# Optimization experiments

Measured on AMD Instinct MI355X. Metric: run time of the kernel, lower is better.

The kernel has to match this reference:

```python
import jax, jax.numpy as jnp
import numpy as np

B, N, M = 2, 512, 8192
DIM, CTX, H, DH, MULT = 1024, 512, 16, 64, 4
INNER = H * DH


def layernorm(x, scale, bias, eps=1e-5):
    mu = x.mean(-1, keepdims=True)
    var = ((x - mu) ** 2).mean(-1, keepdims=True)
    return (x - mu) / jnp.sqrt(var + eps) * scale + bias


def rotate_half(x):
    # interleaved pairs: (..., d) -> (..., d/2, 2), (x1, x2) -> (-x2, x1)
    xr = x.reshape(x.shape[:-1] + (-1, 2))
    x1, x2 = xr[..., 0], xr[..., 1]
    return jnp.stack((-x2, x1), axis=-1).reshape(x.shape)


def apply_rope(freqs, x):
    # freqs: [b, seq, dh] -> [b, 1, seq, dh]; x: [b, h, seq, dh]
    f = freqs[:, None, :, :]
    return x * jnp.cos(f) + rotate_half(x) * jnp.sin(f)


def setup_inputs() -> dict:
    key = jax.random.key(0)
    ks = jax.random.split(key, 24)
    s = 0.02
    inp = {
        "x_query": jax.random.normal(ks[0], (B, N, DIM), jnp.float32),
        "x_context": jax.random.normal(ks[1], (B, M, CTX), jnp.float32),
        "rope_q": jax.random.normal(ks[2], (B, N, DH), jnp.float32),
        "rope_ctx": jax.random.normal(ks[3], (B, M, DH), jnp.float32),
        "Wq": jax.random.normal(ks[4], (DIM, INNER), jnp.float32) * s,
        "Wkv": jax.random.normal(ks[5], (CTX, 2 * INNER), jnp.float32) * s,
        "Wo": jax.random.normal(ks[6], (INNER, DIM), jnp.float32) * s,
        "bo": jnp.zeros((DIM,), jnp.float32),
        "ln_q_scale": jnp.ones((DIM,), jnp.float32),
        "ln_q_bias": jnp.zeros((DIM,), jnp.float32),
        "ln_c_scale": jnp.ones((CTX,), jnp.float32),
        "ln_c_bias": jnp.zeros((CTX,), jnp.float32),
        "ffn_ln_scale": jnp.ones((DIM,), jnp.float32),
        "ffn_ln_bias": jnp.zeros((DIM,), jnp.float32),
        "W1": jax.random.normal(ks[7], (DIM, DIM * MULT * 2), jnp.float32) * s,
        "b1": jnp.zeros((DIM * MULT * 2,), jnp.float32),
        "W2": jax.random.normal(ks[8], (DIM * MULT, DIM), jnp.float32) * s,
        "b2": jnp.zeros((DIM,), jnp.float32),
        "attn_mask": jnp.ones((B, M), dtype=bool),
    }
    return inp


def reference(x_query, x_context, rope_q, rope_ctx, Wq, Wkv, Wo, bo,
              ln_q_scale, ln_q_bias, ln_c_scale, ln_c_bias,
              ffn_ln_scale, ffn_ln_bias, W1, b1, W2, b2, attn_mask):
    # --- RotaryCrossAttention ---
    hq = layernorm(x_query, ln_q_scale, ln_q_bias)
    hc = layernorm(x_context, ln_c_scale, ln_c_bias)
    q = (hq @ Wq).reshape(B, N, H, DH).transpose(0, 2, 1, 3)          # b h n d
    kv = hc @ Wkv
    k = kv[..., :INNER].reshape(B, M, H, DH).transpose(0, 2, 1, 3)    # b h m d
    v = kv[..., INNER:].reshape(B, M, H, DH).transpose(0, 2, 1, 3)
    q = apply_rope(rope_q, q)
    k = apply_rope(rope_ctx, k)
    v = apply_rope(rope_ctx, v)  # rotate_value=True
    scale = DH ** -0.5
    scores = jnp.einsum('bhnd,bhmd->bhnm', q, k) * scale
    scores = jnp.where(attn_mask[:, None, None, :], scores, -1e9)
    attn = jax.nn.softmax(scores, axis=-1)
    out = jnp.einsum('bhnm,bhmd->bhnd', attn, v)
    out = apply_rope(-rope_q, out)  # un-rotate values
    out = out.transpose(0, 2, 1, 3).reshape(B, N, INNER)
    out = out @ Wo + bo
    res = x_query + out
    # --- pre-norm GEGLU FeedForward ---
    y = layernorm(res, ffn_ln_scale, ffn_ln_bias)
    u = y @ W1 + b1
    a, g = u[..., :DIM * MULT], u[..., DIM * MULT:]
    z = (a * jax.nn.gelu(g, approximate=False)) @ W2 + b2
    return res + z
```

## Files before the change

kernel.cpp:

```cpp
#include <hip/hip_runtime.h>
#include <hip/hip_bf16.h>
#include <math.h>


typedef __bf16 bf16;
typedef __bf16 bf16x8 __attribute__((ext_vector_type(8)));
typedef float f32x4 __attribute__((ext_vector_type(4)));

#define DEVI static __device__ __forceinline__

union BV {
  uint4 u;
  bf16 b[8];
  bf16x8 v;
};

DEVI float bf2f(bf16 x) { return (float)x; }
DEVI bf16 f2bf(float x) { return (bf16)x; }

DEVI void gload16(const void* g, void* l) {
  __builtin_amdgcn_global_load_lds((const __attribute__((address_space(1))) void*)g,
                                   (__attribute__((address_space(3))) void*)l, 16, 0, 0);
}

// ... 102 lines not shown
    if constexpr (EPI == 7) {
      const int b = bn >> 2;
      const int nblk = (bn & 3) * 128;
#pragma unroll
      for (int it = 0; it < 8; it++) {
        const int id = it * 256 + tid;
        const int hl = id >> 10, rem = id & 1023;
        const int mm = rem >> 3, c = rem & 7;
        const uint4 vv = *(const uint4*)(ot + mm * 272 + hl * 128 + c * 16);
        const int hg = bm * 2 + hl;
        *(uint4*)((bf16*)out0 + ((size_t)(b * 16 + hg) * 512 + nblk + mm) * 64 + c * 8) = vv;
      }
    } else {
      const int b = bn >> 6;
      const int mblk = (bn & 63) * 128;
      if (isK) {
#pragma unroll
        for (int it = 0; it < 8; it++) {
          const int id = it * 256 + tid;
          const int hl = id >> 10, rem = id & 1023;
          const int mm = rem >> 3, c = rem & 7;
          const uint4 vv = *(const uint4*)(ot + mm * 272 + hl * 128 + c * 16);
          const int hg = bm * 2 + hl;
          *(uint4*)((bf16*)out0 + ((size_t)(b * 16 + hg) * 8192 + mblk + mm) * 64 + c * 8) = vv;
        }
      } else {
#pragma unroll
        for (int it = 0; it < 8; it++) {
          const int id = it * 256 + tid;
          const int nl = id >> 4, c = id & 15;
          const uint4 vv = *(const uint4*)(ot + nl * 272 + c * 16);
          const int hg = (bm - 8) * 2 + (nl >> 6);
          const int d = nl & 63;
          *(uint4*)((bf16*)out1 + ((size_t)(b * 16 + hg) * 64 + d) * 8192 + mblk + c * 8) = vv;
        }
      }
    }
  } else {
#pragma unroll
    for (int fm = 0; fm < 4; fm++) {
#pragma unroll
      for (int fn = 0; fn < 4; fn++) {
        const int col = bn * 128 + wn * 64 + fn * 16 + ln15;
#pragma unroll
        for (int j = 0; j < 4; j++) {
          const int row = bm * 128 + wm * 64 + fm * 16 + lh * 4 + j;
          ((bf16*)out0)[((size_t)zidx * Mdim + row) * Ndim + col] = f2bf(acc[fm][fn][j]);
        }
      }
    }
  }
}

__global__ __launch_bounds__(256, 2)
void gemm128_p(const bf16* __restrict__ A, const bf16* __restrict__ Bt,
               int Mdim, int Ndim, int Kdim,
               void* __restrict__ out0) {
  extern __shared__ char smem[];
  const int kpz = Kdim / gridDim.z;
  gemm_body<6>(smem, blockIdx.x, blockIdx.y, blockIdx.z * kpz, kpz, blockIdx.z,
               A, Bt, Mdim, Ndim, Kdim, nullptr, out0, nullptr);
}

__global__ __launch_bounds__(256, 2)
void gemm_kvq(const bf16* __restrict__ WkvT, const bf16* __restrict__ hc,
              const float* __restrict__ cs, bf16* __restrict__ k_buf,
              bf16* __restrict__ v_t, const bf16* __restrict__ hq,
              const bf16* __restrict__ WqT, const float* __restrict__ csq,
              bf16* __restrict__ q_buf) {
  extern __shared__ char smem[];
  const int fid = blockIdx.x;
  if (fid < 64) {
    gemm_body<7>(smem, fid >> 3, fid & 7, 0, 1024, 0,
                 WqT, hq, 1024, 1024, 1024, csq, q_buf, nullptr);
  } else {
    const int t = fid - 64;
    const int bn = (t & 7) * 16 + ((t >> 3) & 15);
    const int bm = t >> 7;
    gemm_body<5>(smem, bm, bn, 0, 512, 0, WkvT, hc, 2048, 16384, 512, cs, k_buf, v_t);
  }
}

__global__ __launch_bounds__(256, 4)
void gemm_geglu(const bf16* __restrict__ A, const bf16* __restrict__ Bt,
                const float* __restrict__ b1, bf16* __restrict__ hg) {
  __shared__ bf16 As[64 * 64];
  __shared__ bf16 Bs[128 * 64];
  const int tid = threadIdx.x;
  const int w = tid >> 6, l = tid & 63;
  const int bm = blockIdx.x, bn = blockIdx.y;
  const int ln15 = l & 15, lh = l >> 4;
  const int sw7 = ln15 & 7;

  const int gcol = ((l & 7) ^ ((l >> 3) & 7)) << 3;
  const bf16* aG = A + (size_t)(bm * 64 + w * 16 + (l >> 3)) * 1024 + gcol;
  bf16* lA = As + (w * 16) * 64;
  const bf16* bG = Bt + (size_t)((w >> 1) * 4096 + bn * 64 + ((w & 1) * 32 + (l >> 3))) * 1024 + gcol;
  bf16* lB = Bs + (w * 32) * 64;

  const f32x4 z4 = {0.f, 0.f, 0.f, 0.f};
  f32x4 acc[2][4];
#pragma unroll
  for (int p = 0; p < 2; p++)
#pragma unroll
    for (int i = 0; i < 4; i++) acc[p][i] = z4;

  const char* Ab = (const char*)As;
  const char* Bb = (const char*)Bs;
  const int arow_b = ln15 * 128;

  for (int k0 = 0; k0 < 1024; k0 += 64) {
#pragma unroll
    for (int gi = 0; gi < 2; gi++)
      gload16(aG + (size_t)(gi * 8) * 1024 + k0, lA + gi * 512);
#pragma unroll
    for (int gi = 0; gi < 4; gi++)
      gload16(bG + (size_t)(gi * 8) * 1024 + k0, lB + gi * 512);
    __syncthreads();
#pragma unroll
    for (int kk = 0; kk < 2; kk++) {
      const int gx = (((kk << 2) | lh) ^ sw7) << 4;
      bf16x8 af[4], bfr[2];
#pragma unroll
      for (int f = 0; f < 4; f++) {
        BV t0;
        t0.u = *(const uint4*)(Ab + arow_b + f * 2048 + gx);
        af[f] = t0.v;
      }
#pragma unroll
      for (int p = 0; p < 2; p++) {
        const int cu = p * 64 + w * 16 + ln15;
        BV t0;
        t0.u = *(const uint4*)(Bb + cu * 128 + gx);
        bfr[p] = t0.v;
      }
#pragma unroll
      for (int fm = 0; fm < 4; fm++)
#pragma unroll
        for (int p = 0; p < 2; p++)
          acc[p][fm] = __builtin_amdgcn_mfma_f32_16x16x32_bf16(af[fm], bfr[p], acc[p][fm], 0, 0, 0);
    }
    __syncthreads();
  }

  const int col = bn * 64 + w * 16 + ln15;
  const float ba = b1[col], bg = b1[4096 + col];
#pragma unroll
  for (int fm = 0; fm < 4; fm++) {
#pragma unroll
    for (int j = 0; j < 4; j++) {
      const int row = bm * 64 + fm * 16 + lh * 4 + j;
      const float a = acc[0][fm][j] + ba;
      const float g = acc[1][fm][j] + bg;
      const float ge = 0.5f * g * (1.f + erff(g * 0.70710678118f));
      hg[(size_t)row * 4096 + col] = f2bf(a * ge);
    }
  }
}

template <int S>
__global__ __launch_bounds__(256)
void combine_res_ln(const bf16* __restrict__ part, const float* __restrict__ bias,
                    const float* __restrict__ resid, float* __restrict__ out,
                    const float* __restrict__ lnsc, const float* __restrict__ lnbi,
                    bf16* __restrict__ yout) {
  __shared__ float r0[4], r1[4];
  const int row = blockIdx.x, tid = threadIdx.x;
  const int wv = tid >> 6, l = tid & 63;
  const size_t i4 = (size_t)row * 1024 + tid * 4;
  const int col = tid * 4;
  float4 s = {0.f, 0.f, 0.f, 0.f};
#pragma unroll
  for (int p = 0; p < S; p++) {
    union { uint2 u; bf16 bb[4]; } t;
    t.u = *(const uint2*)(part + (size_t)p * 1048576 + i4);
    s.x += bf2f(t.bb[0]); s.y += bf2f(t.bb[1]);
    s.z += bf2f(t.bb[2]); s.w += bf2f(t.bb[3]);
  }
  const float4 bv = *(const float4*)(bias + col);
  const float4 rv = *(const float4*)(resid + i4);
  s.x += bv.x + rv.x; s.y += bv.y + rv.y; s.z += bv.z + rv.z; s.w += bv.w + rv.w;
  *(float4*)(out + i4) = s;
  float sm = s.x + s.y + s.z + s.w;
  float ss = s.x * s.x + s.y * s.y + s.z * s.z + s.w * s.w;
#pragma unroll
  for (int off = 1; off < 64; off <<= 1) { sm += __shfl_xor(sm, off); ss += __shfl_xor(ss, off); }
  if (l == 0) { r0[wv] = sm; r1[wv] = ss; }
  __syncthreads();
  sm = r0[0] + r0[1] + r0[2] + r0[3];
  ss = r1[0] + r1[1] + r1[2] + r1[3];
  const float mu = sm * (1.f / 1024.f);
  const float rstd = rsqrtf(ss * (1.f / 1024.f) - mu * mu + 1e-5f);
  const float4 scv = *(const float4*)(lnsc + col);
  const float4 biv = *(const float4*)(lnbi + col);
  union { uint2 u; bf16 bb[4]; } y;
  y.bb[0] = f2bf((s.x - mu) * rstd * scv.x + biv.x);
  y.bb[1] = f2bf((s.y - mu) * rstd * scv.y + biv.y);
  y.bb[2] = f2bf((s.z - mu) * rstd * scv.z + biv.z);
  y.bb[3] = f2bf((s.w - mu) * rstd * scv.w + biv.w);
  *(uint2*)(yout + i4) = y.u;
}

template <int S>
__global__ __launch_bounds__(256)
void combine_res_bf16(const bf16* __restrict__ part, const float* __restrict__ bias,
                      const float* __restrict__ resid, float* __restrict__ out) {
  const size_t i4 = ((size_t)blockIdx.x * 256 + threadIdx.x) * 4;
  float4 s = {0.f, 0.f, 0.f, 0.f};
#pragma unroll
  for (int p = 0; p < S; p++) {
    union { uint2 u; bf16 bb[4]; } t;
    t.u = *(const uint2*)(part + (size_t)p * 1048576 + i4);
    s.x += bf2f(t.bb[0]); s.y += bf2f(t.bb[1]);
    s.z += bf2f(t.bb[2]); s.w += bf2f(t.bb[3]);
  }
  const int col = (int)(i4 & 1023);
  const float4 bv = *(const float4*)(bias + col);
  const float4 rv = *(const float4*)(resid + i4);
  s.x += bv.x + rv.x; s.y += bv.y + rv.y; s.z += bv.z + rv.z; s.w += bv.w + rv.w;
  *(float4*)(out + i4) = s;
}

__global__ __launch_bounds__(256, 4)
void attn_kernel(const bf16* __restrict__ q_buf, const bf16* __restrict__ k_buf,
                 const bf16* __restrict__ v_t, bf16* __restrict__ opart,
                 float* __restrict__ lpart) {
  __shared__ bf16 Ks[2][64 * 64];
  __shared__ bf16 Vs[2][64 * 64];
  __shared__ bf16 Ps[4][16][64];
  const int id = blockIdx.x;
  const int sp = id >> 7, qt = (id >> 5) & 3, bh = id & 31;
  const int tid = threadIdx.x;
  const int w = tid >> 6, l = tid & 63;
  const int ln15 = l & 15, lh = l >> 4;

  const bf16* qbase = q_buf + ((size_t)bh * 512 + qt * 128 + w * 32) * 64;
  const bf16* kbase = k_buf + (size_t)bh * 8192 * 64;
  const bf16* vbase = v_t + (size_t)bh * 64 * 8192;

  bf16x8 aq[2][2];
#pragma unroll
  for (int rh = 0; rh < 2; rh++) {
    const bf16* qp = qbase + (size_t)(rh * 16 + ln15) * 64 + lh * 8;
    BV t0; t0.u = *(const uint4*)qp; aq[rh][0] = t0.v;
    BV t1; t1.u = *(const uint4*)(qp + 32); aq[rh][1] = t1.v;
  }

  const f32x4 z4 = {0.f, 0.f, 0.f, 0.f};
  f32x4 o[2][4];
#pragma unroll
  for (int rh = 0; rh < 2; rh++)
#pragma unroll
    for (int fd = 0; fd < 4; fd++) o[rh][fd] = z4;
  f32x4 ol[2] = {z4, z4};

  BV ones;
#pragma unroll
  for (int i = 0; i < 8; i++) ones.b[i] = f2bf(1.0f);

  const int srow0 = ((w << 1) | 0) * 8 + (l >> 3);
  const int srow1 = ((w << 1) | 1) * 8 + (l >> 3);
  const int slot = l & 7;
  const int g0 = (slot ^ (srow0 & 7)) << 3;
  const int g1 = (slot ^ (srow1 & 7)) << 3;
  const bf16* k0p = kbase + (size_t)srow0 * 64 + g0;
  const bf16* k1p = kbase + (size_t)srow1 * 64 + g1;
  const bf16* v0p = vbase + (size_t)srow0 * 8192 + g0;
  const bf16* v1p = vbase + (size_t)srow1 * 8192 + g1;
  const int lo0 = ((w << 1) | 0) * 512;
  const int lo1 = ((w << 1) | 1) * 512;

  const int mt0 = sp * 16;
  auto STAGE = [&](int b, int mt) {
    const size_t mo = (size_t)mt * 4096;
    const size_t mv = (size_t)mt * 64;
    gload16(k0p + mo, Ks[b] + lo0);
    gload16(k1p + mo, Ks[b] + lo1);
    gload16(v0p + mv, Vs[b] + lo0);
    gload16(v1p + mv, Vs[b] + lo1);
  };

  STAGE(0, mt0);
  __syncthreads();

  char* pbase = (char*)&Ps[w][0][0];
  const int swq = ln15 & 7;

  for (int i = 0; i < 16; i++) {
    const int cur = i & 1;
    if (i < 15) STAGE(cur ^ 1, mt0 + i + 1);

    const char* Kb = (const char*)Ks[cur];
    const char* Vb = (const char*)Vs[cur];

    f32x4 sf[2][4];
#pragma unroll
    for (int rh = 0; rh < 2; rh++)
#pragma unroll
      for (int fn = 0; fn < 4; fn++) sf[rh][fn] = z4;
    __builtin_amdgcn_s_setprio(1);
#pragma unroll
    for (int fn = 0; fn < 4; fn++) {
      const int mrow = fn * 16 + ln15;
      const int sw = mrow & 7;
      BV t0; t0.u = *(const uint4*)(Kb + mrow * 128 + ((lh ^ sw) << 4));
      BV t1; t1.u = *(const uint4*)(Kb + mrow * 128 + (((lh + 4) ^ sw) << 4));
      sf[0][fn] = __builtin_amdgcn_mfma_f32_16x16x32_bf16(t0.v, aq[0][0], sf[0][fn], 0, 0, 0);
      sf[0][fn] = __builtin_amdgcn_mfma_f32_16x16x32_bf16(t1.v, aq[0][1], sf[0][fn], 0, 0, 0);
      sf[1][fn] = __builtin_amdgcn_mfma_f32_16x16x32_bf16(t0.v, aq[1][0], sf[1][fn], 0, 0, 0);
      sf[1][fn] = __builtin_amdgcn_mfma_f32_16x16x32_bf16(t1.v, aq[1][1], sf[1][fn], 0, 0, 0);
    }
    __builtin_amdgcn_s_setprio(0);

    BV pa[2][2];
#pragma unroll
    for (int rh = 0; rh < 2; rh++) {
      char* prow = pbase + ln15 * 128;
#pragma unroll
      for (int fn = 0; fn < 4; fn++) {
        const float p0 = exp2f(sf[rh][fn][0]);
        const float p1 = exp2f(sf[rh][fn][1]);
        const float p2 = exp2f(sf[rh][fn][2]);
        const float p3 = exp2f(sf[rh][fn][3]);
        union { uint2 u; bf16 bb[4]; } pk;
        pk.bb[0] = f2bf(p0); pk.bb[1] = f2bf(p1);
        pk.bb[2] = f2bf(p2); pk.bb[3] = f2bf(p3);
        const int G = (fn * 2 + (lh >> 1)) ^ swq;
        *(uint2*)(prow + G * 16 + (lh & 1) * 8) = pk.u;
      }
#pragma unroll
      for (int mh = 0; mh < 2; mh++) {
        const int R = ((mh << 2) | lh) ^ swq;
        pa[rh][mh].u = *(const uint4*)(pbase + ln15 * 128 + (R << 4));
      }
    }

    __builtin_amdgcn_s_setprio(1);
#pragma unroll
    for (int mh = 0; mh < 2; mh++) {
      ol[0] = __builtin_amdgcn_mfma_f32_16x16x32_bf16(pa[0][mh].v, ones.v, ol[0], 0, 0, 0);
      ol[1] = __builtin_amdgcn_mfma_f32_16x16x32_bf16(pa[1][mh].v, ones.v, ol[1], 0, 0, 0);
#pragma unroll
      for (int fd = 0; fd < 4; fd++) {
        const int drow = fd * 16 + ln15;
        BV bv; bv.u = *(const uint4*)(Vb + drow * 128 + ((((mh << 2) | lh) ^ (drow & 7)) << 4));
        o[0][fd] = __builtin_amdgcn_mfma_f32_16x16x32_bf16(pa[0][mh].v, bv.v, o[0][fd], 0, 0, 0);
        o[1][fd] = __builtin_amdgcn_mfma_f32_16x16x32_bf16(pa[1][mh].v, bv.v, o[1][fd], 0, 0, 0);
      }
    }
    __builtin_amdgcn_s_setprio(0);
    __syncthreads();
  }

#pragma unroll
  for (int rh = 0; rh < 2; rh++) {
    if (ln15 == 0) {
#pragma unroll
      for (int j = 0; j < 4; j++)
        lpart[(size_t)id * 128 + w * 32 + rh * 16 + lh * 4 + j] = ol[rh][j];
    }
    bf16* op = opart + (size_t)id * 8192 + (w * 32 + rh * 16) * 64;
#pragma unroll
    for (int fd = 0; fd < 4; fd++)
#pragma unroll
      for (int j = 0; j < 4; j++)
        op[(lh * 4 + j) * 64 + fd * 16 + ln15] = f2bf(o[rh][fd][j]);
  }
}

DEVI void tr_tile(bf16 (*t)[74], const float* __restrict__ in, bf16* __restrict__ out,
                  int R, int C, int ct, int rt, int tid) {
  const int tr = tid >> 2, tc = (tid & 3) << 4;
  {
    const float* src = in + (size_t)(rt * 64 + tr) * C + ct * 64 + tc;
    const float4 a0 = *(const float4*)src;
    const float4 a1 = *(const float4*)(src + 4);
    const float4 a2 = *(const float4*)(src + 8);
    const float4 a3 = *(const float4*)(src + 12);
    t[tr][tc + 0] = f2bf(a0.x);  t[tr][tc + 1] = f2bf(a0.y);
    t[tr][tc + 2] = f2bf(a0.z);  t[tr][tc + 3] = f2bf(a0.w);
    t[tr][tc + 4] = f2bf(a1.x);  t[tr][tc + 5] = f2bf(a1.y);
    t[tr][tc + 6] = f2bf(a1.z);  t[tr][tc + 7] = f2bf(a1.w);
    t[tr][tc + 8] = f2bf(a2.x);  t[tr][tc + 9] = f2bf(a2.y);
    t[tr][tc + 10] = f2bf(a2.z); t[tr][tc + 11] = f2bf(a2.w);
    t[tr][tc + 12] = f2bf(a3.x); t[tr][tc + 13] = f2bf(a3.y);
    t[tr][tc + 14] = f2bf(a3.z); t[tr][tc + 15] = f2bf(a3.w);
  }
  __syncthreads();
  {
    BV a0, a1;
#pragma unroll
    for (int i = 0; i < 8; i++) { a0.b[i] = t[tc + i][tr]; a1.b[i] = t[tc + 8 + i][tr]; }
    bf16* dst = out + (size_t)(ct * 64 + tr) * R + rt * 64 + tc;
    *(uint4*)dst = a0.u;
    *(uint4*)(dst + 8) = a1.u;
  }
}

__global__ __launch_bounds__(256)
void combine_tr_kernel(const bf16* __restrict__ opart, const float* __restrict__ lpart,
                       const float* __restrict__ ct_, const float* __restrict__ st_,
                       bf16* __restrict__ o_lin,
                       const float* __restrict__ W1, bf16* __restrict__ W1T,
                       const float* __restrict__ W2, bf16* __restrict__ W2T) {
  int id = blockIdx.x;
  if (id < 1024) {
    const size_t i4 = ((size_t)id * 256 + threadIdx.x) * 4;
    const int d4 = (int)(i4 & 63);
    const int row = (int)(i4 >> 6);
    const int qg = row & 511;
    const int bh = row >> 9;
    const int qt = qg >> 7, ql = qg & 127;
    const int id0 = (qt << 5) | bh;
    float4 acc = {0.f, 0.f, 0.f, 0.f};
    float L = 0.f;
#pragma unroll
    for (int sp = 0; sp < 8; sp++) {
      const int pid = (sp << 7) | id0;
      union { uint2 u; bf16 bb[4]; } t;
      t.u = *(const uint2*)(opart + (size_t)pid * 8192 + ql * 64 + d4);
      acc.x += bf2f(t.bb[0]); acc.y += bf2f(t.bb[1]);
      acc.z += bf2f(t.bb[2]); acc.w += bf2f(t.bb[3]);
      L += lpart[(size_t)pid * 128 + ql];
    }
    const float inv = 1.f / L;
    const float x0 = acc.x * inv, x1 = acc.y * inv, x2 = acc.z * inv, x3 = acc.w * inv;
    const int b = bh >> 4, h = bh & 15, n = qg;
    const size_t fo = (((size_t)b * 512 + n) * 64) + d4;
    const float4 cv = *(const float4*)(ct_ + fo);
    const float4 sv = *(const float4*)(st_ + fo);
    union { uint2 u; bf16 bb[4]; } o;
    o.bb[0] = f2bf(x0 * cv.x + x1 * sv.x);
    o.bb[1] = f2bf(x1 * cv.y - x0 * sv.y);
    o.bb[2] = f2bf(x2 * cv.z + x3 * sv.z);
    o.bb[3] = f2bf(x3 * cv.w - x2 * sv.w);
    *(uint2*)(o_lin + (((size_t)b * 512 + n) * 1024) + h * 64 + d4) = o.u;
  } else {
    __shared__ bf16 t[64][74];
    id -= 1024;
    if (id < 2048) {
      tr_tile(t, W1, W1T, 1024, 8192, id & 127, id >> 7, threadIdx.x);
    } else {
      id -= 2048;
      tr_tile(t, W2, W2T, 4096, 1024, id & 15, id >> 4, threadIdx.x);
    }
  }
}

template <int W>
DEVI void ln_row(const float* __restrict__ xr, const float* __restrict__ sc,
                 const float* __restrict__ bi, bf16* __restrict__ outr,
                 int tid, float* r0, float* r1) {
  constexpr int PER = W / 256;
  const int w = tid >> 6, l = tid & 63;
  float v[PER];
  if constexpr (PER == 4) {
    const float4 t = *(const float4*)(xr + tid * 4);
    v[0] = t.x; v[1] = t.y; v[2] = t.z; v[3] = t.w;
  } else {
    const float2 t = *(const float2*)(xr + tid * 2);
    v[0] = t.x; v[1] = t.y;
  }
  float s = 0.f, ss = 0.f;
#pragma unroll
  for (int i = 0; i < PER; i++) { s += v[i]; ss += v[i] * v[i]; }
#pragma unroll
  for (int off = 1; off < 64; off <<= 1) { s += __shfl_xor(s, off); ss += __shfl_xor(ss, off); }
  if (l == 0) { r0[w] = s; r1[w] = ss; }
  __syncthreads();
  s = r0[0] + r0[1] + r0[2] + r0[3];
  ss = r1[0] + r1[1] + r1[2] + r1[3];
  const float mu = s * (1.f / W);
  const float rstd = rsqrtf(ss * (1.f / W) - mu * mu + 1e-5f);
  if constexpr (PER == 4) {
    union { uint2 u; bf16 b[4]; } t;
#pragma unroll
    for (int i = 0; i < 4; i++) {
      const int c = tid * 4 + i;
      t.b[i] = f2bf((v[i] - mu) * rstd * sc[c] + bi[c]);
    }
    *(uint2*)(outr + tid * 4) = t.u;
  } else {
    union { unsigned u; bf16 b[2]; } t;
#pragma unroll
    for (int i = 0; i < 2; i++) {
      const int c = tid * 2 + i;
      t.b[i] = f2bf((v[i] - mu) * rstd * sc[c] + bi[c]);
    }
    *(unsigned*)(outr + tid * 2) = t.u;
  }
}

__global__ __launch_bounds__(256)
void setup_kernel(const float* __restrict__ Wq, bf16* __restrict__ WqT,
                  const float* __restrict__ Wkv, bf16* __restrict__ WkvT,
                  const float* __restrict__ Wo, bf16* __restrict__ WoT,
                  const float* __restrict__ fq, float* __restrict__ cq,
                  float* __restrict__ sq_, unsigned* __restrict__ csq,
                  const float* __restrict__ fc, unsigned* __restrict__ cs,
// ... 70 lines not shown
  const float* lnf_s = (const float*)d_in[12];
  const float* lnf_b = (const float*)d_in[13];
  const float* W1 = (const float*)d_in[14];
  const float* b1 = (const float*)d_in[15];
  const float* W2 = (const float*)d_in[16];
  const float* b2 = (const float*)d_in[17];

  char* ws = (char*)d_ws;
  size_t off = 0;
  auto alloc = [&](size_t bytes) {
    char* p = ws + off;
    off += (bytes + 255) & ~(size_t)255;
    return p;
  };

  bf16* WqT = (bf16*)alloc((size_t)1048576 * 2);
  bf16* WkvT = (bf16*)alloc((size_t)1048576 * 2);
  bf16* WoT = (bf16*)alloc((size_t)1048576 * 2);
  bf16* hq = (bf16*)alloc((size_t)1048576 * 2);
  bf16* q_buf = (bf16*)alloc((size_t)1048576 * 2);
  float* cosq = (float*)alloc((size_t)65536 * 4);
  float* sinq = (float*)alloc((size_t)65536 * 4);
  unsigned* csq = (unsigned*)alloc((size_t)65536 * 4);
  unsigned* cs_ctx = (unsigned*)alloc((size_t)1048576 * 4);
  bf16* o_lin = (bf16*)alloc((size_t)1048576 * 2);
  float* res = (float*)alloc((size_t)1048576 * 4);
  bf16* ybuf = (bf16*)alloc((size_t)1048576 * 2);
  float* lpart = (float*)alloc((size_t)131072 * 4);
  bf16* hc = (bf16*)alloc((size_t)8388608 * 2);
  bf16* k_buf = (bf16*)alloc((size_t)16777216 * 2);
  bf16* W1T = k_buf;
  bf16* W2T = k_buf + 8388608;
  bf16* hg = k_buf + 8388608 + 4194304;
  char* regB = alloc((size_t)16777216 * 2);
  bf16* opart = (bf16*)regB;
  bf16* pwo = (bf16*)regB;
  bf16* pf2 = (bf16*)regB;
  bf16* v_tb = (bf16*)alloc((size_t)16777216 * 2);
  (void)ws_size;

  const int SH = 32768;
  const int SH5 = 34816;

  setup_kernel<<<22528, 256, 0, stream>>>(Wq, WqT, Wkv, WkvT, Wo, WoT,
                                          rope_q, cosq, sinq, csq, rope_ctx, cs_ctx,
                                          x_query, lnq_s, lnq_b, hq,
                                          x_context, lnc_s, lnc_b, hc);

  gemm_kvq<<<2112, 256, SH5, stream>>>(WkvT, hc, (const float*)cs_ctx,
                                       k_buf, v_tb, hq, WqT,
                                       (const float*)csq, q_buf);

  attn_kernel<<<1024, 256, 0, stream>>>(q_buf, k_buf, v_tb, opart, lpart);
  combine_tr_kernel<<<4096, 256, 0, stream>>>(opart, lpart, cosq, sinq, o_lin,
                                              W1, W1T, W2, W2T);

  gemm128_p<<<dim3(8, 8, 4), 256, SH, stream>>>(o_lin, WoT, 1024, 1024, 1024, pwo);
  combine_res_ln<4><<<1024, 256, 0, stream>>>(pwo, bo, x_query, res, lnf_s, lnf_b, ybuf);

  gemm_geglu<<<dim3(16, 64), 256, 0, stream>>>(ybuf, W1T, b1, hg);
  gemm128_p<<<dim3(8, 8, 8), 256, SH, stream>>>(hg, W2T, 1024, 1024, 4096, pf2);
  combine_res_bf16<8><<<1024, 256, 0, stream>>>(pf2, b2, res, (float*)d_out);
}
```

Baseline: 206.7 us.

## Move W1/W2 transposes from attention combine into split-K Wo GEMM launch

```diff
diff --git a/kernel.cpp b/kernel.cpp
--- a/kernel.cpp
+++ b/kernel.cpp
@@ -178,322 +178,6 @@
   }
 }
 
-__global__ __launch_bounds__(256, 2)
-void gemm128_p(const bf16* __restrict__ A, const bf16* __restrict__ Bt,
-               int Mdim, int Ndim, int Kdim,
-               void* __restrict__ out0) {
-  extern __shared__ char smem[];
-  const int kpz = Kdim / gridDim.z;
-  gemm_body<6>(smem, blockIdx.x, blockIdx.y, blockIdx.z * kpz, kpz, blockIdx.z,
-               A, Bt, Mdim, Ndim, Kdim, nullptr, out0, nullptr);
-}
-
-__global__ __launch_bounds__(256, 2)
-void gemm_kvq(const bf16* __restrict__ WkvT, const bf16* __restrict__ hc,
-              const float* __restrict__ cs, bf16* __restrict__ k_buf,
-              bf16* __restrict__ v_t, const bf16* __restrict__ hq,
-              const bf16* __restrict__ WqT, const float* __restrict__ csq,
-              bf16* __restrict__ q_buf) {
-  extern __shared__ char smem[];
-  const int fid = blockIdx.x;
-  if (fid < 64) {
-    gemm_body<7>(smem, fid >> 3, fid & 7, 0, 1024, 0,
-                 WqT, hq, 1024, 1024, 1024, csq, q_buf, nullptr);
-  } else {
-    const int t = fid - 64;
-    const int bn = (t & 7) * 16 + ((t >> 3) & 15);
-    const int bm = t >> 7;
-    gemm_body<5>(smem, bm, bn, 0, 512, 0, WkvT, hc, 2048, 16384, 512, cs, k_buf, v_t);
-  }
-}
-
-__global__ __launch_bounds__(256, 4)
-void gemm_geglu(const bf16* __restrict__ A, const bf16* __restrict__ Bt,
-                const float* __restrict__ b1, bf16* __restrict__ hg) {
-  __shared__ bf16 As[64 * 64];
-  __shared__ bf16 Bs[128 * 64];
-  const int tid = threadIdx.x;
-  const int w = tid >> 6, l = tid & 63;
-  const int bm = blockIdx.x, bn = blockIdx.y;
-  const int ln15 = l & 15, lh = l >> 4;
-  const int sw7 = ln15 & 7;
-
-  const int gcol = ((l & 7) ^ ((l >> 3) & 7)) << 3;
-  const bf16* aG = A + (size_t)(bm * 64 + w * 16 + (l >> 3)) * 1024 + gcol;
-  bf16* lA = As + (w * 16) * 64;
-  const bf16* bG = Bt + (size_t)((w >> 1) * 4096 + bn * 64 + ((w & 1) * 32 + (l >> 3))) * 1024 + gcol;
-  bf16* lB = Bs + (w * 32) * 64;
-
-  const f32x4 z4 = {0.f, 0.f, 0.f, 0.f};
-  f32x4 acc[2][4];
-#pragma unroll
-  for (int p = 0; p < 2; p++)
-#pragma unroll
-    for (int i = 0; i < 4; i++) acc[p][i] = z4;
-
-  const char* Ab = (const char*)As;
-  const char* Bb = (const char*)Bs;
-  const int arow_b = ln15 * 128;
-
-  for (int k0 = 0; k0 < 1024; k0 += 64) {
-#pragma unroll
-    for (int gi = 0; gi < 2; gi++)
-      gload16(aG + (size_t)(gi * 8) * 1024 + k0, lA + gi * 512);
-#pragma unroll
-    for (int gi = 0; gi < 4; gi++)
-      gload16(bG + (size_t)(gi * 8) * 1024 + k0, lB + gi * 512);
-    __syncthreads();
-#pragma unroll
-    for (int kk = 0; kk < 2; kk++) {
-      const int gx = (((kk << 2) | lh) ^ sw7) << 4;
-      bf16x8 af[4], bfr[2];
-#pragma unroll
-      for (int f = 0; f < 4; f++) {
-        BV t0;
-        t0.u = *(const uint4*)(Ab + arow_b + f * 2048 + gx);
-        af[f] = t0.v;
-      }
-#pragma unroll
-      for (int p = 0; p < 2; p++) {
-        const int cu = p * 64 + w * 16 + ln15;
-        BV t0;
-        t0.u = *(const uint4*)(Bb + cu * 128 + gx);
-        bfr[p] = t0.v;
-      }
-#pragma unroll
-      for (int fm = 0; fm < 4; fm++)
-#pragma unroll
-        for (int p = 0; p < 2; p++)
-          acc[p][fm] = __builtin_amdgcn_mfma_f32_16x16x32_bf16(af[fm], bfr[p], acc[p][fm], 0, 0, 0);
-    }
-    __syncthreads();
-  }
-
-  const int col = bn * 64 + w * 16 + ln15;
-  const float ba = b1[col], bg = b1[4096 + col];
-#pragma unroll
-  for (int fm = 0; fm < 4; fm++) {
-#pragma unroll
-    for (int j = 0; j < 4; j++) {
-      const int row = bm * 64 + fm * 16 + lh * 4 + j;
-      const float a = acc[0][fm][j] + ba;
-      const float g = acc[1][fm][j] + bg;
-      const float ge = 0.5f * g * (1.f + erff(g * 0.70710678118f));
-      hg[(size_t)row * 4096 + col] = f2bf(a * ge);
-    }
-  }
-}
-
-template <int S>
-__global__ __launch_bounds__(256)
-void combine_res_ln(const bf16* __restrict__ part, const float* __restrict__ bias,
-                    const float* __restrict__ resid, float* __restrict__ out,
-                    const float* __restrict__ lnsc, const float* __restrict__ lnbi,
-                    bf16* __restrict__ yout) {
-  __shared__ float r0[4], r1[4];
-  const int row = blockIdx.x, tid = threadIdx.x;
-  const int wv = tid >> 6, l = tid & 63;
-  const size_t i4 = (size_t)row * 1024 + tid * 4;
-  const int col = tid * 4;
-  float4 s = {0.f, 0.f, 0.f, 0.f};
-#pragma unroll
-  for (int p = 0; p < S; p++) {
-    union { uint2 u; bf16 bb[4]; } t;
-    t.u = *(const uint2*)(part + (size_t)p * 1048576 + i4);
-    s.x += bf2f(t.bb[0]); s.y += bf2f(t.bb[1]);
-    s.z += bf2f(t.bb[2]); s.w += bf2f(t.bb[3]);
-  }
-  const float4 bv = *(const float4*)(bias + col);
-  const float4 rv = *(const float4*)(resid + i4);
-  s.x += bv.x + rv.x; s.y += bv.y + rv.y; s.z += bv.z + rv.z; s.w += bv.w + rv.w;
-  *(float4*)(out + i4) = s;
-  float sm = s.x + s.y + s.z + s.w;
-  float ss = s.x * s.x + s.y * s.y + s.z * s.z + s.w * s.w;
-#pragma unroll
-  for (int off = 1; off < 64; off <<= 1) { sm += __shfl_xor(sm, off); ss += __shfl_xor(ss, off); }
-  if (l == 0) { r0[wv] = sm; r1[wv] = ss; }
-  __syncthreads();
-  sm = r0[0] + r0[1] + r0[2] + r0[3];
-  ss = r1[0] + r1[1] + r1[2] + r1[3];
-  const float mu = sm * (1.f / 1024.f);
-  const float rstd = rsqrtf(ss * (1.f / 1024.f) - mu * mu + 1e-5f);
-  const float4 scv = *(const float4*)(lnsc + col);
-  const float4 biv = *(const float4*)(lnbi + col);
-  union { uint2 u; bf16 bb[4]; } y;
-  y.bb[0] = f2bf((s.x - mu) * rstd * scv.x + biv.x);
-  y.bb[1] = f2bf((s.y - mu) * rstd * scv.y + biv.y);
-  y.bb[2] = f2bf((s.z - mu) * rstd * scv.z + biv.z);
-  y.bb[3] = f2bf((s.w - mu) * rstd * scv.w + biv.w);
-  *(uint2*)(yout + i4) = y.u;
-}
-
-template <int S>
-__global__ __launch_bounds__(256)
-void combine_res_bf16(const bf16* __restrict__ part, const float* __restrict__ bias,
-                      const float* __restrict__ resid, float* __restrict__ out) {
-  const size_t i4 = ((size_t)blockIdx.x * 256 + threadIdx.x) * 4;
-  float4 s = {0.f, 0.f, 0.f, 0.f};
-#pragma unroll
-  for (int p = 0; p < S; p++) {
-    union { uint2 u; bf16 bb[4]; } t;
-    t.u = *(const uint2*)(part + (size_t)p * 1048576 + i4);
-    s.x += bf2f(t.bb[0]); s.y += bf2f(t.bb[1]);
-    s.z += bf2f(t.bb[2]); s.w += bf2f(t.bb[3]);
-  }
-  const int col = (int)(i4 & 1023);
-  const float4 bv = *(const float4*)(bias + col);
-  const float4 rv = *(const float4*)(resid + i4);
-  s.x += bv.x + rv.x; s.y += bv.y + rv.y; s.z += bv.z + rv.z; s.w += bv.w + rv.w;
-  *(float4*)(out + i4) = s;
-}
-
-__global__ __launch_bounds__(256, 4)
-void attn_kernel(const bf16* __restrict__ q_buf, const bf16* __restrict__ k_buf,
-                 const bf16* __restrict__ v_t, bf16* __restrict__ opart,
-                 float* __restrict__ lpart) {
-  __shared__ bf16 Ks[2][64 * 64];
-  __shared__ bf16 Vs[2][64 * 64];
-  __shared__ bf16 Ps[4][16][64];
-  const int id = blockIdx.x;
-  const int sp = id >> 7, qt = (id >> 5) & 3, bh = id & 31;
-  const int tid = threadIdx.x;
-  const int w = tid >> 6, l = tid & 63;
-  const int ln15 = l & 15, lh = l >> 4;
-
-  const bf16* qbase = q_buf + ((size_t)bh * 512 + qt * 128 + w * 32) * 64;
-  const bf16* kbase = k_buf + (size_t)bh * 8192 * 64;
-  const bf16* vbase = v_t + (size_t)bh * 64 * 8192;
-
-  bf16x8 aq[2][2];
-#pragma unroll
-  for (int rh = 0; rh < 2; rh++) {
-    const bf16* qp = qbase + (size_t)(rh * 16 + ln15) * 64 + lh * 8;
-    BV t0; t0.u = *(const uint4*)qp; aq[rh][0] = t0.v;
-    BV t1; t1.u = *(const uint4*)(qp + 32); aq[rh][1] = t1.v;
-  }
-
-  const f32x4 z4 = {0.f, 0.f, 0.f, 0.f};
-  f32x4 o[2][4];
-#pragma unroll
-  for (int rh = 0; rh < 2; rh++)
-#pragma unroll
-    for (int fd = 0; fd < 4; fd++) o[rh][fd] = z4;
-  f32x4 ol[2] = {z4, z4};
-
-  BV ones;
-#pragma unroll
-  for (int i = 0; i < 8; i++) ones.b[i] = f2bf(1.0f);
-
-  const int srow0 = ((w << 1) | 0) * 8 + (l >> 3);
-  const int srow1 = ((w << 1) | 1) * 8 + (l >> 3);
-  const int slot = l & 7;
-  const int g0 = (slot ^ (srow0 & 7)) << 3;
-  const int g1 = (slot ^ (srow1 & 7)) << 3;
-  const bf16* k0p = kbase + (size_t)srow0 * 64 + g0;
-  const bf16* k1p = kbase + (size_t)srow1 * 64 + g1;
-  const bf16* v0p = vbase + (size_t)srow0 * 8192 + g0;
-  const bf16* v1p = vbase + (size_t)srow1 * 8192 + g1;
-  const int lo0 = ((w << 1) | 0) * 512;
-  const int lo1 = ((w << 1) | 1) * 512;
-
-  const int mt0 = sp * 16;
-  auto STAGE = [&](int b, int mt) {
-    const size_t mo = (size_t)mt * 4096;
-    const size_t mv = (size_t)mt * 64;
-    gload16(k0p + mo, Ks[b] + lo0);
-    gload16(k1p + mo, Ks[b] + lo1);
-    gload16(v0p + mv, Vs[b] + lo0);
-    gload16(v1p + mv, Vs[b] + lo1);
-  };
-
-  STAGE(0, mt0);
-  __syncthreads();
-
-  char* pbase = (char*)&Ps[w][0][0];
-  const int swq = ln15 & 7;
-
-  for (int i = 0; i < 16; i++) {
-    const int cur = i & 1;
-    if (i < 15) STAGE(cur ^ 1, mt0 + i + 1);
-
-    const char* Kb = (const char*)Ks[cur];
-    const char* Vb = (const char*)Vs[cur];
-
-    f32x4 sf[2][4];
-#pragma unroll
-    for (int rh = 0; rh < 2; rh++)
-#pragma unroll
-      for (int fn = 0; fn < 4; fn++) sf[rh][fn] = z4;
-    __builtin_amdgcn_s_setprio(1);
-#pragma unroll
-    for (int fn = 0; fn < 4; fn++) {
-      const int mrow = fn * 16 + ln15;
-      const int sw = mrow & 7;
-      BV t0; t0.u = *(const uint4*)(Kb + mrow * 128 + ((lh ^ sw) << 4));
-      BV t1; t1.u = *(const uint4*)(Kb + mrow * 128 + (((lh + 4) ^ sw) << 4));
-      sf[0][fn] = __builtin_amdgcn_mfma_f32_16x16x32_bf16(t0.v, aq[0][0], sf[0][fn], 0, 0, 0);
-      sf[0][fn] = __builtin_amdgcn_mfma_f32_16x16x32_bf16(t1.v, aq[0][1], sf[0][fn], 0, 0, 0);
-      sf[1][fn] = __builtin_amdgcn_mfma_f32_16x16x32_bf16(t0.v, aq[1][0], sf[1][fn], 0, 0, 0);
-      sf[1][fn] = __builtin_amdgcn_mfma_f32_16x16x32_bf16(t1.v, aq[1][1], sf[1][fn], 0, 0, 0);
-    }
-    __builtin_amdgcn_s_setprio(0);
-
-    BV pa[2][2];
-#pragma unroll
-    for (int rh = 0; rh < 2; rh++) {
-      char* prow = pbase + ln15 * 128;
-#pragma unroll
-      for (int fn = 0; fn < 4; fn++) {
-        const float p0 = exp2f(sf[rh][fn][0]);
-        const float p1 = exp2f(sf[rh][fn][1]);
-        const float p2 = exp2f(sf[rh][fn][2]);
-        const float p3 = exp2f(sf[rh][fn][3]);
-        union { uint2 u; bf16 bb[4]; } pk;
-        pk.bb[0] = f2bf(p0); pk.bb[1] = f2bf(p1);
-        pk.bb[2] = f2bf(p2); pk.bb[3] = f2bf(p3);
-        const int G = (fn * 2 + (lh >> 1)) ^ swq;
-        *(uint2*)(prow + G * 16 + (lh & 1) * 8) = pk.u;
-      }
-#pragma unroll
-      for (int mh = 0; mh < 2; mh++) {
-        const int R = ((mh << 2) | lh) ^ swq;
-        pa[rh][mh].u = *(const uint4*)(pbase + ln15 * 128 + (R << 4));
-      }
-    }
-
-    __builtin_amdgcn_s_setprio(1);
-#pragma unroll
-    for (int mh = 0; mh < 2; mh++) {
-      ol[0] = __builtin_amdgcn_mfma_f32_16x16x32_bf16(pa[0][mh].v, ones.v, ol[0], 0, 0, 0);
-      ol[1] = __builtin_amdgcn_mfma_f32_16x16x32_bf16(pa[1][mh].v, ones.v, ol[1], 0, 0, 0);
-#pragma unroll
-      for (int fd = 0; fd < 4; fd++) {
-        const int drow = fd * 16 + ln15;
-        BV bv; bv.u = *(const uint4*)(Vb + drow * 128 + ((((mh << 2) | lh) ^ (drow & 7)) << 4));
-        o[0][fd] = __builtin_amdgcn_mfma_f32_16x16x32_bf16(pa[0][mh].v, bv.v, o[0][fd], 0, 0, 0);
-        o[1][fd] = __builtin_amdgcn_mfma_f32_16x16x32_bf16(pa[1][mh].v, bv.v, o[1][fd], 0, 0, 0);
-      }
-    }
-    __builtin_amdgcn_s_setprio(0);
-    __syncthreads();
-  }
-
-#pragma unroll
-  for (int rh = 0; rh < 2; rh++) {
-    if (ln15 == 0) {
-#pragma unroll
-      for (int j = 0; j < 4; j++)
-        lpart[(size_t)id * 128 + w * 32 + rh * 16 + lh * 4 + j] = ol[rh][j];
-    }
-    bf16* op = opart + (size_t)id * 8192 + (w * 32 + rh * 16) * 64;
-#pragma unroll
-    for (int fd = 0; fd < 4; fd++)
-#pragma unroll
-      for (int j = 0; j < 4; j++)
-        op[(lh * 4 + j) * 64 + fd * 16 + ln15] = f2bf(o[rh][fd][j]);
-  }
-}
-
 DEVI void tr_tile(bf16 (*t)[74], const float* __restrict__ in, bf16* __restrict__ out,
                   int R, int C, int ct, int rt, int tid) {
   const int tr = tid >> 2, tc = (tid & 3) << 4;
@@ -523,54 +207,379 @@
   }
 }
 
+__global__ __launch_bounds__(256, 2)
+void gemm_kvq(const bf16* __restrict__ WkvT, const bf16* __restrict__ hc,
+              const float* __restrict__ cs, bf16* __restrict__ k_buf,
+              bf16* __restrict__ v_t, const bf16* __restrict__ hq,
+              const bf16* __restrict__ WqT, const float* __restrict__ csq,
+              bf16* __restrict__ q_buf) {
+  extern __shared__ char smem[];
+  const int fid = blockIdx.x;
+  if (fid < 64) {
+    gemm_body<7>(smem, fid >> 3, fid & 7, 0, 1024, 0,
+                 WqT, hq, 1024, 1024, 1024, csq, q_buf, nullptr);
+  } else {
+    const int t = fid - 64;
+    const int bn = (t & 7) * 16 + ((t >> 3) & 15);
+    const int bm = t >> 7;
+    gemm_body<5>(smem, bm, bn, 0, 512, 0, WkvT, hc, 2048, 16384, 512, cs, k_buf, v_t);
+  }
+}
+
+__global__ __launch_bounds__(256, 2)
+void gemm_wo_tr(const bf16* __restrict__ o_lin, const bf16* __restrict__ WoT,
+                bf16* __restrict__ pwo,
+                const float* __restrict__ W1, bf16* __restrict__ W1T,
+                const float* __restrict__ W2, bf16* __restrict__ W2T) {
+  extern __shared__ char smem[];
+  int fid = blockIdx.x;
+  if (fid < 512) {
+    const int z = fid >> 6, bm = (fid >> 3) & 7, bn = fid & 7;
+    gemm_body<6>(smem, bm, bn, z * 128, 128, z,
+                 o_lin, WoT, 1024, 1024, 1024, nullptr, pwo, nullptr);
+  } else {
+    bf16 (*t)[74] = (bf16(*)[74])smem;
+    fid -= 512;
+    if (fid < 2048) {
+      tr_tile(t, W1, W1T, 1024, 8192, fid & 127, fid >> 7, threadIdx.x);
+    } else {
+      fid -= 2048;
+      tr_tile(t, W2, W2T, 4096, 1024, fid & 15, fid >> 4, threadIdx.x);
+    }
+  }
+}
+
+__global__ __launch_bounds__(256, 2)
+void gemm128_p(const bf16* __restrict__ A, const bf16* __restrict__ Bt,
+               int Mdim, int Ndim, int Kdim,
+               void* __restrict__ out0) {
+  extern __shared__ char smem[];
+  const int kpz = Kdim / gridDim.z;
+  gemm_body<6>(smem, blockIdx.x, blockIdx.y, blockIdx.z * kpz, kpz, blockIdx.z,
+               A, Bt, Mdim, Ndim, Kdim, nullptr, out0, nullptr);
+}
+
+__global__ __launch_bounds__(256, 4)
+void gemm_geglu(const bf16* __restrict__ A, const bf16* __restrict__ Bt,
+                const float* __restrict__ b1, bf16* __restrict__ hg) {
+  __shared__ bf16 As[64 * 64];
+  __shared__ bf16 Bs[128 * 64];
+  const int tid = threadIdx.x;
+  const int w = tid >> 6, l = tid & 63;
+  const int bm = blockIdx.x, bn = blockIdx.y;
+  const int ln15 = l & 15, lh = l >> 4;
+  const int sw7 = ln15 & 7;
+
+  const int gcol = ((l & 7) ^ ((l >> 3) & 7)) << 3;
+  const bf16* aG = A + (size_t)(bm * 64 + w * 16 + (l >> 3)) * 1024 + gcol;
+  bf16* lA = As + (w * 16) * 64;
+  const bf16* bG = Bt + (size_t)((w >> 1) * 4096 + bn * 64 + ((w & 1) * 32 + (l >> 3))) * 1024 + gcol;
+  bf16* lB = Bs + (w * 32) * 64;
+
+  const f32x4 z4 = {0.f, 0.f, 0.f, 0.f};
+  f32x4 acc[2][4];
+#pragma unroll
+  for (int p = 0; p < 2; p++)
+#pragma unroll
+    for (int i = 0; i < 4; i++) acc[p][i] = z4;
+
+  const char* Ab = (const char*)As;
+  const char* Bb = (const char*)Bs;
+  const int arow_b = ln15 * 128;
+
+  for (int k0 = 0; k0 < 1024; k0 += 64) {
+#pragma unroll
+    for (int gi = 0; gi < 2; gi++)
+      gload16(aG + (size_t)(gi * 8) * 1024 + k0, lA + gi * 512);
+#pragma unroll
+    for (int gi = 0; gi < 4; gi++)
+      gload16(bG + (size_t)(gi * 8) * 1024 + k0, lB + gi * 512);
+    __syncthreads();
+#pragma unroll
+    for (int kk = 0; kk < 2; kk++) {
+      const int gx = (((kk << 2) | lh) ^ sw7) << 4;
+      bf16x8 af[4], bfr[2];
+#pragma unroll
+      for (int f = 0; f < 4; f++) {
+        BV t0;
+        t0.u = *(const uint4*)(Ab + arow_b + f * 2048 + gx);
+        af[f] = t0.v;
+      }
+#pragma unroll
+      for (int p = 0; p < 2; p++) {
+        const int cu = p * 64 + w * 16 + ln15;
+        BV t0;
+        t0.u = *(const uint4*)(Bb + cu * 128 + gx);
+        bfr[p] = t0.v;
+      }
+#pragma unroll
+      for (int fm = 0; fm < 4; fm++)
+#pragma unroll
+        for (int p = 0; p < 2; p++)
+          acc[p][fm] = __builtin_amdgcn_mfma_f32_16x16x32_bf16(af[fm], bfr[p], acc[p][fm], 0, 0, 0);
+    }
+    __syncthreads();
+  }
+
+  const int col = bn * 64 + w * 16 + ln15;
+  const float ba = b1[col], bg = b1[4096 + col];
+#pragma unroll
+  for (int fm = 0; fm < 4; fm++) {
+#pragma unroll
+    for (int j = 0; j < 4; j++) {
+      const int row = bm * 64 + fm * 16 + lh * 4 + j;
+      const float a = acc[0][fm][j] + ba;
+      const float g = acc[1][fm][j] + bg;
+      const float ge = 0.5f * g * (1.f + erff(g * 0.70710678118f));
+      hg[(size_t)row * 4096 + col] = f2bf(a * ge);
+    }
+  }
+}
+
+template <int S>
 __global__ __launch_bounds__(256)
-void combine_tr_kernel(const bf16* __restrict__ opart, const float* __restrict__ lpart,
-                       const float* __restrict__ ct_, const float* __restrict__ st_,
-                       bf16* __restrict__ o_lin,
-                       const float* __restrict__ W1, bf16* __restrict__ W1T,
-                       const float* __restrict__ W2, bf16* __restrict__ W2T) {
-  int id = blockIdx.x;
-  if (id < 1024) {
-    const size_t i4 = ((size_t)id * 256 + threadIdx.x) * 4;
-    const int d4 = (int)(i4 & 63);
-    const int row = (int)(i4 >> 6);
-    const int qg = row & 511;
-    const int bh = row >> 9;
-    const int qt = qg >> 7, ql = qg & 127;
-    const int id0 = (qt << 5) | bh;
-    float4 acc = {0.f, 0.f, 0.f, 0.f};
-    float L = 0.f;
-#pragma unroll
-    for (int sp = 0; sp < 8; sp++) {
-      const int pid = (sp << 7) | id0;
-      union { uint2 u; bf16 bb[4]; } t;
-      t.u = *(const uint2*)(opart + (size_t)pid * 8192 + ql * 64 + d4);
-      acc.x += bf2f(t.bb[0]); acc.y += bf2f(t.bb[1]);
-      acc.z += bf2f(t.bb[2]); acc.w += bf2f(t.bb[3]);
-      L += lpart[(size_t)pid * 128 + ql];
-    }
-    const float inv = 1.f / L;
-    const float x0 = acc.x * inv, x1 = acc.y * inv, x2 = acc.z * inv, x3 = acc.w * inv;
-    const int b = bh >> 4, h = bh & 15, n = qg;
-    const size_t fo = (((size_t)b * 512 + n) * 64) + d4;
-    const float4 cv = *(const float4*)(ct_ + fo);
-    const float4 sv = *(const float4*)(st_ + fo);
-    union { uint2 u; bf16 bb[4]; } o;
-    o.bb[0] = f2bf(x0 * cv.x + x1 * sv.x);
-    o.bb[1] = f2bf(x1 * cv.y - x0 * sv.y);
-    o.bb[2] = f2bf(x2 * cv.z + x3 * sv.z);
-    o.bb[3] = f2bf(x3 * cv.w - x2 * sv.w);
-    *(uint2*)(o_lin + (((size_t)b * 512 + n) * 1024) + h * 64 + d4) = o.u;
-  } else {
-    __shared__ bf16 t[64][74];
-    id -= 1024;
-    if (id < 2048) {
-      tr_tile(t, W1, W1T, 1024, 8192, id & 127, id >> 7, threadIdx.x);
-    } else {
-      id -= 2048;
-      tr_tile(t, W2, W2T, 4096, 1024, id & 15, id >> 4, threadIdx.x);
-    }
-  }
+void combine_res_ln(const bf16* __restrict__ part, const float* __restrict__ bias,
+                    const float* __restrict__ resid, float* __restrict__ out,
+                    const float* __restrict__ lnsc, const float* __restrict__ lnbi,
+                    bf16* __restrict__ yout) {
+  __shared__ float r0[4], r1[4];
+  const int row = blockIdx.x, tid = threadIdx.x;
+  const int wv = tid >> 6, l = tid & 63;
+  const size_t i4 = (size_t)row * 1024 + tid * 4;
+  const int col = tid * 4;
+  float4 s = {0.f, 0.f, 0.f, 0.f};
+#pragma unroll
+  for (int p = 0; p < S; p++) {
+    union { uint2 u; bf16 bb[4]; } t;
+    t.u = *(const uint2*)(part + (size_t)p * 1048576 + i4);
+    s.x += bf2f(t.bb[0]); s.y += bf2f(t.bb[1]);
+    s.z += bf2f(t.bb[2]); s.w += bf2f(t.bb[3]);
+  }
+  const float4 bv = *(const float4*)(bias + col);
+  const float4 rv = *(const float4*)(resid + i4);
+  s.x += bv.x + rv.x; s.y += bv.y + rv.y; s.z += bv.z + rv.z; s.w += bv.w + rv.w;
+  *(float4*)(out + i4) = s;
+  float sm = s.x + s.y + s.z + s.w;
+  float ss = s.x * s.x + s.y * s.y + s.z * s.z + s.w * s.w;
+#pragma unroll
+  for (int off = 1; off < 64; off <<= 1) { sm += __shfl_xor(sm, off); ss += __shfl_xor(ss, off); }
+  if (l == 0) { r0[wv] = sm; r1[wv] = ss; }
+  __syncthreads();
+  sm = r0[0] + r0[1] + r0[2] + r0[3];
+  ss = r1[0] + r1[1] + r1[2] + r1[3];
+  const float mu = sm * (1.f / 1024.f);
+  const float rstd = rsqrtf(ss * (1.f / 1024.f) - mu * mu + 1e-5f);
+  const float4 scv = *(const float4*)(lnsc + col);
+  const float4 biv = *(const float4*)(lnbi + col);
+  union { uint2 u; bf16 bb[4]; } y;
+  y.bb[0] = f2bf((s.x - mu) * rstd * scv.x + biv.x);
+  y.bb[1] = f2bf((s.y - mu) * rstd * scv.y + biv.y);
+  y.bb[2] = f2bf((s.z - mu) * rstd * scv.z + biv.z);
+  y.bb[3] = f2bf((s.w - mu) * rstd * scv.w + biv.w);
+  *(uint2*)(yout + i4) = y.u;
+}
+
+template <int S>
+__global__ __launch_bounds__(256)
+void combine_res_bf16(const bf16* __restrict__ part, const float* __restrict__ bias,
+                      const float* __restrict__ resid, float* __restrict__ out) {
+  const size_t i4 = ((size_t)blockIdx.x * 256 + threadIdx.x) * 4;
+  float4 s = {0.f, 0.f, 0.f, 0.f};
+#pragma unroll
+  for (int p = 0; p < S; p++) {
+    union { uint2 u; bf16 bb[4]; } t;
+    t.u = *(const uint2*)(part + (size_t)p * 1048576 + i4);
+    s.x += bf2f(t.bb[0]); s.y += bf2f(t.bb[1]);
+    s.z += bf2f(t.bb[2]); s.w += bf2f(t.bb[3]);
+  }
+  const int col = (int)(i4 & 1023);
+  const float4 bv = *(const float4*)(bias + col);
+  const float4 rv = *(const float4*)(resid + i4);
+  s.x += bv.x + rv.x; s.y += bv.y + rv.y; s.z += bv.z + rv.z; s.w += bv.w + rv.w;
+  *(float4*)(out + i4) = s;
+}
+
+__global__ __launch_bounds__(256, 4)
+void attn_kernel(const bf16* __restrict__ q_buf, const bf16* __restrict__ k_buf,
+                 const bf16* __restrict__ v_t, bf16* __restrict__ opart,
+                 float* __restrict__ lpart) {
+  __shared__ bf16 Ks[2][64 * 64];
+  __shared__ bf16 Vs[2][64 * 64];
+  __shared__ bf16 Ps[4][16][64];
+  const int id = blockIdx.x;
+  const int sp = id >> 7, qt = (id >> 5) & 3, bh = id & 31;
+  const int tid = threadIdx.x;
+  const int w = tid >> 6, l = tid & 63;
+  const int ln15 = l & 15, lh = l >> 4;
+
+  const bf16* qbase = q_buf + ((size_t)bh * 512 + qt * 128 + w * 32) * 64;
+  const bf16* kbase = k_buf + (size_t)bh * 8192 * 64;
+  const bf16* vbase = v_t + (size_t)bh * 64 * 8192;
+
+  bf16x8 aq[2][2];
+#pragma unroll
+  for (int rh = 0; rh < 2; rh++) {
+    const bf16* qp = qbase + (size_t)(rh * 16 + ln15) * 64 + lh * 8;
+    BV t0; t0.u = *(const uint4*)qp; aq[rh][0] = t0.v;
+    BV t1; t1.u = *(const uint4*)(qp + 32); aq[rh][1] = t1.v;
+  }
+
+  const f32x4 z4 = {0.f, 0.f, 0.f, 0.f};
+  f32x4 o[2][4];
+#pragma unroll
+  for (int rh = 0; rh < 2; rh++)
+#pragma unroll
+    for (int fd = 0; fd < 4; fd++) o[rh][fd] = z4;
+  f32x4 ol[2] = {z4, z4};
+
+  BV ones;
+#pragma unroll
+  for (int i = 0; i < 8; i++) ones.b[i] = f2bf(1.0f);
+
+  const int srow0 = ((w << 1) | 0) * 8 + (l >> 3);
+  const int srow1 = ((w << 1) | 1) * 8 + (l >> 3);
+  const int slot = l & 7;
+  const int g0 = (slot ^ (srow0 & 7)) << 3;
+  const int g1 = (slot ^ (srow1 & 7)) << 3;
+  const bf16* k0p = kbase + (size_t)srow0 * 64 + g0;
+  const bf16* k1p = kbase + (size_t)srow1 * 64 + g1;
+  const bf16* v0p = vbase + (size_t)srow0 * 8192 + g0;
+  const bf16* v1p = vbase + (size_t)srow1 * 8192 + g1;
+  const int lo0 = ((w << 1) | 0) * 512;
+  const int lo1 = ((w << 1) | 1) * 512;
+
+  const int mt0 = sp * 16;
+  auto STAGE = [&](int b, int mt) {
+    const size_t mo = (size_t)mt * 4096;
+    const size_t mv = (size_t)mt * 64;
+    gload16(k0p + mo, Ks[b] + lo0);
+    gload16(k1p + mo, Ks[b] + lo1);
+    gload16(v0p + mv, Vs[b] + lo0);
+    gload16(v1p + mv, Vs[b] + lo1);
+  };
+
+  STAGE(0, mt0);
+  __syncthreads();
+
+  char* pbase = (char*)&Ps[w][0][0];
+  const int swq = ln15 & 7;
+
+  for (int i = 0; i < 16; i++) {
+    const int cur = i & 1;
+    if (i < 15) STAGE(cur ^ 1, mt0 + i + 1);
+
+    const char* Kb = (const char*)Ks[cur];
+    const char* Vb = (const char*)Vs[cur];
+
+    f32x4 sf[2][4];
+#pragma unroll
+    for (int rh = 0; rh < 2; rh++)
+#pragma unroll
+      for (int fn = 0; fn < 4; fn++) sf[rh][fn] = z4;
+    __builtin_amdgcn_s_setprio(1);
+#pragma unroll
+    for (int fn = 0; fn < 4; fn++) {
+      const int mrow = fn * 16 + ln15;
+      const int sw = mrow & 7;
+      BV t0; t0.u = *(const uint4*)(Kb + mrow * 128 + ((lh ^ sw) << 4));
+      BV t1; t1.u = *(const uint4*)(Kb + mrow * 128 + (((lh + 4) ^ sw) << 4));
+      sf[0][fn] = __builtin_amdgcn_mfma_f32_16x16x32_bf16(t0.v, aq[0][0], sf[0][fn], 0, 0, 0);
+      sf[0][fn] = __builtin_amdgcn_mfma_f32_16x16x32_bf16(t1.v, aq[0][1], sf[0][fn], 0, 0, 0);
+      sf[1][fn] = __builtin_amdgcn_mfma_f32_16x16x32_bf16(t0.v, aq[1][0], sf[1][fn], 0, 0, 0);
+      sf[1][fn] = __builtin_amdgcn_mfma_f32_16x16x32_bf16(t1.v, aq[1][1], sf[1][fn], 0, 0, 0);
+    }
+    __builtin_amdgcn_s_setprio(0);
+
+    BV pa[2][2];
+#pragma unroll
+    for (int rh = 0; rh < 2; rh++) {
+      char* prow = pbase + ln15 * 128;
+#pragma unroll
+      for (int fn = 0; fn < 4; fn++) {
+        const float p0 = exp2f(sf[rh][fn][0]);
+        const float p1 = exp2f(sf[rh][fn][1]);
+        const float p2 = exp2f(sf[rh][fn][2]);
+        const float p3 = exp2f(sf[rh][fn][3]);
+        union { uint2 u; bf16 bb[4]; } pk;
+        pk.bb[0] = f2bf(p0); pk.bb[1] = f2bf(p1);
+        pk.bb[2] = f2bf(p2); pk.bb[3] = f2bf(p3);
+        const int G = (fn * 2 + (lh >> 1)) ^ swq;
+        *(uint2*)(prow + G * 16 + (lh & 1) * 8) = pk.u;
+      }
+#pragma unroll
+      for (int mh = 0; mh < 2; mh++) {
+        const int R = ((mh << 2) | lh) ^ swq;
+        pa[rh][mh].u = *(const uint4*)(pbase + ln15 * 128 + (R << 4));
+      }
+    }
+
+    __builtin_amdgcn_s_setprio(1);
+#pragma unroll
+    for (int mh = 0; mh < 2; mh++) {
+      ol[0] = __builtin_amdgcn_mfma_f32_16x16x32_bf16(pa[0][mh].v, ones.v, ol[0], 0, 0, 0);
+      ol[1] = __builtin_amdgcn_mfma_f32_16x16x32_bf16(pa[1][mh].v, ones.v, ol[1], 0, 0, 0);
+#pragma unroll
+      for (int fd = 0; fd < 4; fd++) {
+        const int drow = fd * 16 + ln15;
+        BV bv; bv.u = *(const uint4*)(Vb + drow * 128 + ((((mh << 2) | lh) ^ (drow & 7)) << 4));
+        o[0][fd] = __builtin_amdgcn_mfma_f32_16x16x32_bf16(pa[0][mh].v, bv.v, o[0][fd], 0, 0, 0);
+        o[1][fd] = __builtin_amdgcn_mfma_f32_16x16x32_bf16(pa[1][mh].v, bv.v, o[1][fd], 0, 0, 0);
+      }
+    }
+    __builtin_amdgcn_s_setprio(0);
+    __syncthreads();
+  }
+
+#pragma unroll
+  for (int rh = 0; rh < 2; rh++) {
+    if (ln15 == 0) {
+#pragma unroll
+      for (int j = 0; j < 4; j++)
+        lpart[(size_t)id * 128 + w * 32 + rh * 16 + lh * 4 + j] = ol[rh][j];
+    }
+    bf16* op = opart + (size_t)id * 8192 + (w * 32 + rh * 16) * 64;
+#pragma unroll
+    for (int fd = 0; fd < 4; fd++)
+#pragma unroll
+      for (int j = 0; j < 4; j++)
+        op[(lh * 4 + j) * 64 + fd * 16 + ln15] = f2bf(o[rh][fd][j]);
+  }
+}
+
+__global__ __launch_bounds__(256)
+void attn_combine_kernel(const bf16* __restrict__ opart, const float* __restrict__ lpart,
+                         const float* __restrict__ ct_, const float* __restrict__ st_,
+                         bf16* __restrict__ o_lin) {
+  const size_t i4 = ((size_t)blockIdx.x * 256 + threadIdx.x) * 4;
+  const int d4 = (int)(i4 & 63);
+  const int row = (int)(i4 >> 6);
+  const int qg = row & 511;
+  const int bh = row >> 9;
+  const int qt = qg >> 7, ql = qg & 127;
+  const int id0 = (qt << 5) | bh;
+  float4 acc = {0.f, 0.f, 0.f, 0.f};
+  float L = 0.f;
+#pragma unroll
+  for (int sp = 0; sp < 8; sp++) {
+    const int pid = (sp << 7) | id0;
+    union { uint2 u; bf16 bb[4]; } t;
+    t.u = *(const uint2*)(opart + (size_t)pid * 8192 + ql * 64 + d4);
+    acc.x += bf2f(t.bb[0]); acc.y += bf2f(t.bb[1]);
+    acc.z += bf2f(t.bb[2]); acc.w += bf2f(t.bb[3]);
+    L += lpart[(size_t)pid * 128 + ql];
+  }
+  const float inv = 1.f / L;
+  const float x0 = acc.x * inv, x1 = acc.y * inv, x2 = acc.z * inv, x3 = acc.w * inv;
+  const int b = bh >> 4, h = bh & 15, n = qg;
+  const size_t fo = (((size_t)b * 512 + n) * 64) + d4;
+  const float4 cv = *(const float4*)(ct_ + fo);
+  const float4 sv = *(const float4*)(st_ + fo);
+  union { uint2 u; bf16 bb[4]; } o;
+  o.bb[0] = f2bf(x0 * cv.x + x1 * sv.x);
+  o.bb[1] = f2bf(x1 * cv.y - x0 * sv.y);
+  o.bb[2] = f2bf(x2 * cv.z + x3 * sv.z);
+  o.bb[3] = f2bf(x3 * cv.w - x2 * sv.w);
+  *(uint2*)(o_lin + (((size_t)b * 512 + n) * 1024) + h * 64 + d4) = o.u;
 }
 
 template <int W>
@@ -747,11 +756,10 @@
                                        (const float*)csq, q_buf);
 
   attn_kernel<<<1024, 256, 0, stream>>>(q_buf, k_buf, v_tb, opart, lpart);
-  combine_tr_kernel<<<4096, 256, 0, stream>>>(opart, lpart, cosq, sinq, o_lin,
-                                              W1, W1T, W2, W2T);
-
-  gemm128_p<<<dim3(8, 8, 4), 256, SH, stream>>>(o_lin, WoT, 1024, 1024, 1024, pwo);
-  combine_res_ln<4><<<1024, 256, 0, stream>>>(pwo, bo, x_query, res, lnf_s, lnf_b, ybuf);
+  attn_combine_kernel<<<1024, 256, 0, stream>>>(opart, lpart, cosq, sinq, o_lin);
+
+  gemm_wo_tr<<<3584, 256, SH, stream>>>(o_lin, WoT, pwo, W1, W1T, W2, W2T);
+  combine_res_ln<8><<<1024, 256, 0, stream>>>(pwo, bo, x_query, res, lnf_s, lnf_b, ybuf);
 
   gemm_geglu<<<dim3(16, 64), 256, 0, stream>>>(ybuf, W1T, b1, hg);
   gemm128_p<<<dim3(8, 8, 8), 256, SH, stream>>>(hg, W2T, 1024, 1024, 4096, pf2);
```

Result: no change. 207.6 us (+0.4%).
